# Optimization experiments

Hardware: AMD Instinct MI355X
Metric: run time of the kernel (lower is better)

The kernel has to match this reference:

```python
import jax, jax.numpy as jnp
import numpy as np

B, S, D, E = 2, 2048, 1024, 16  # batch, cutoff (seq), dmodel, n_experts


def setup_inputs() -> dict:
    key = jax.random.key(0)
    k = jax.random.split(key, 6)
    scale = 1.0 / np.sqrt(D)
    return {
        "x": jax.random.normal(k[0], (B, S, D), dtype=jnp.float32),
        "gate": jax.random.normal(k[1], (D, E), dtype=jnp.float32) * scale,
        "W1": jax.random.normal(k[2], (E, D, D), dtype=jnp.float32) * scale,  # lin1: Linear(dmodel, dmodel*E), split per expert
        "b1": jnp.zeros((E, D), dtype=jnp.float32),
        "W2": jax.random.normal(k[3], (E, D, D), dtype=jnp.float32) * scale,  # lin2: Linear(dmodel*E, dmodel), split per expert
        "b2": jnp.zeros((D,), dtype=jnp.float32),
        "topk": 256,
    }


def reference(x, gate, W1, b1, W2, b2, topk):
    # Expert-choice gating: softmax over the token (cutoff) axis per expert.
    logits = jnp.einsum("bsd,de->bse", x, gate)            # (B, S, E)
    probs = jax.nn.softmax(logits, axis=1)                  # softmax over tokens
    # Each expert selects its top-k tokens.
    g, idx = jax.lax.top_k(jnp.swapaxes(probs, 1, 2), topk)  # (B, E, k)
    # Gather selected tokens: (B, E, k, D)
    xin = jnp.take_along_axis(x[:, None, :, :], idx[..., None], axis=2)
    # Per-expert 2-layer FFN (hidden size = dmodel, per width = dmodel*n_experts)
    h = jax.nn.relu(jnp.einsum("bekd,edf->bekf", xin, W1) + b1[None, :, None, :])
    out = jnp.einsum("bekf,efd->bekd", h, W2) + b2           # (B, E, k, D)
    weighted = out * g[..., None]
    # Scatter-add back to token positions.
    y = jnp.zeros_like(x)
    b_idx = jnp.arange(x.shape[0])[:, None, None]            # (B, 1, 1)
    y = y.at[b_idx, idx].add(weighted)
    return y
```

## Files before the change

### kernel.cpp

```cpp
#include <hip/hip_runtime.h>
#include <stdint.h>
#include <math.h>

constexpr int CB = 2;
constexpr int CS = 2048;
constexpr int CD = 1024;
constexpr int CE = 16;
constexpr int CK = 256;

typedef short bf16x8 __attribute__((ext_vector_type(8)));
typedef float f32x4 __attribute__((ext_vector_type(4)));

typedef __attribute__((address_space(1))) const unsigned int gu32;
typedef __attribute__((address_space(3))) unsigned int lu32;

__device__ __forceinline__ void async16(const void* g, void* l) {
    __builtin_amdgcn_global_load_lds((gu32*)g, (lu32*)l, 16, 0, 0);
}

__device__ inline unsigned short f2bf(float f) {
    union { float f; uint32_t u; } v; v.f = f;
    uint32_t u = v.u;
    uint32_t r = (u + 0x7FFFu + ((u >> 16) & 1u)) >> 16;
    return (unsigned short)r;
}

__global__ __launch_bounds__(256)
void logits_kernel(const float* __restrict__ x,
                   const float* __restrict__ gate,
                   float* __restrict__ logits) {
    const int tid = threadIdx.x;
    const int wid = tid >> 6, l = tid & 63;
    const int bs = blockIdx.x * 4 + wid;
    const float* xr = x + (size_t)bs * CD;
    float acc[CE];
#pragma unroll
    for (int e = 0; e < CE; e++) acc[e] = 0.0f;
#pragma unroll
    for (int i = 0; i < 4; i++) {
        const int d0 = i * 256 + l * 4;
        const f32x4 xv = *(const f32x4*)(xr + d0);
#pragma unroll
        for (int j = 0; j < 4; j++) {
            const f32x4* g4 = (const f32x4*)(gate + (size_t)(d0 + j) * CE);
#pragma unroll
            for (int c = 0; c < 4; c++) {
                const f32x4 gv = g4[c];
#pragma unroll
                for (int u = 0; u < 4; u++) acc[c * 4 + u] += xv[j] * gv[u];
            }
        }
    }
#pragma unroll
    for (int e = 0; e < CE; e++) {
        float v = acc[e];
#pragma unroll
        for (int o = 32; o > 0; o >>= 1) v += __shfl_down(v, o);
        if (l == 0) logits[(size_t)bs * CE + e] = v;
    }
}

__global__ void topk_kernel(const float* __restrict__ logits,
                            int* __restrict__ idx_out,
                            float* __restrict__ g_out) {
    const int be = blockIdx.x;
    const int b = be >> 4, e = be & 15;
    const int tid = threadIdx.x;
    const int lane = tid & 63, wid = tid >> 6;

    __shared__ float redf[4];
    __shared__ int hist[256];
    __shared__ int wsum[4];
    __shared__ int sh_bin, sh_rank;
    __shared__ int scnt, eqc;
    __shared__ int eqbuf[CS];

    float lv[8], p[8];
    unsigned int uv[8];
#pragma unroll
    for (int j = 0; j < 8; j++) {
        const int s = tid + j * 256;
        lv[j] = logits[((size_t)(b * CS + s)) * CE + e];
    }
    float m = lv[0];
#pragma unroll
    for (int j = 1; j < 8; j++) m = fmaxf(m, lv[j]);
#pragma unroll
    for (int o = 32; o > 0; o >>= 1) m = fmaxf(m, __shfl_down(m, o));
    if (lane == 0) redf[wid] = m;
    __syncthreads();
    m = fmaxf(fmaxf(redf[0], redf[1]), fmaxf(redf[2], redf[3]));
    __syncthreads();
    float lsum = 0.0f;
#pragma unroll
    for (int j = 0; j < 8; j++) {
        p[j] = expf(lv[j] - m);
        uv[j] = __float_as_uint(p[j]);
        lsum += p[j];
    }
#pragma unroll
    for (int o = 32; o > 0; o >>= 1) lsum += __shfl_down(lsum, o);
    if (lane == 0) redf[wid] = lsum;
    __syncthreads();
    const float total = redf[0] + redf[1] + redf[2] + redf[3];
    const float inv_total = 1.0f / total;

    unsigned int prefix = 0;
    int kneed = CK;
    for (int pass = 0; pass < 4; pass++) {
        const int shift = 24 - 8 * pass;
        __syncthreads();
        hist[tid] = 0;
        __syncthreads();
        const unsigned int hmask = (pass == 0) ? 0u : (0xFFFFFFFFu << (shift + 8));
#pragma unroll
        for (int j = 0; j < 8; j++)
            if ((uv[j] & hmask) == prefix)
                atomicAdd(&hist[(uv[j] >> shift) & 255], 1);
        __syncthreads();
        const int own = hist[tid];
        int s = own;
#pragma unroll
        for (int o = 1; o < 64; o <<= 1) {
            int t = __shfl_down(s, o);
            if (lane + o < 64) s += t;
        }
        if (lane == 0) wsum[wid] = s;
        __syncthreads();
        int above = 0;
        for (int ww = wid + 1; ww < 4; ww++) above += wsum[ww];
        const int incl = s + above;
        if (incl >= kneed && (incl - own) < kneed) {
            sh_bin = tid;
            sh_rank = kneed - (incl - own);
        }
        __syncthreads();
        prefix |= ((unsigned int)sh_bin) << shift;
        kneed = sh_rank;
    }
    const unsigned int v = prefix;
    const int quota = kneed;

    if (tid == 0) { scnt = 0; eqc = 0; }
    __syncthreads();
#pragma unroll
    for (int j = 0; j < 8; j++) {
        const int s = tid + j * 256;
        if (uv[j] > v) {
            const int pos = atomicAdd(&scnt, 1);
            idx_out[be * CK + pos] = s;
            g_out[be * CK + pos] = p[j] * inv_total;
        } else if (uv[j] == v) {
            const int pos = atomicAdd(&eqc, 1);
            eqbuf[pos] = s;
        }
    }
    __syncthreads();
    if (tid == 0) {
        const int cgt = scnt;
        const int n = eqc;
        const float gv = __uint_as_float(v) * inv_total;
        if (n > quota) {
            for (int i = 0; i < quota; i++) {
                int mn = i;
                for (int k2 = i + 1; k2 < n; k2++)
                    if (eqbuf[k2] < eqbuf[mn]) mn = k2;
                const int t2 = eqbuf[i]; eqbuf[i] = eqbuf[mn]; eqbuf[mn] = t2;
            }
        }
        for (int i = 0; i < quota; i++) {
            idx_out[be * CK + cgt + i] = eqbuf[i];
            g_out[be * CK + cgt + i] = gv;
        }
    }
}

__global__ void gather_kernel(const float* __restrict__ x,
                              const int* __restrict__ idx_ws,
                              unsigned short* __restrict__ xinbuf) {
    const int row = blockIdx.x;
    const int be = row >> 8;
    const int b = be >> 4;
    const int tok = idx_ws[row];
    const int c0 = threadIdx.x * 4;
    const f32x4 f = *(const f32x4*)(x + ((size_t)b * CS + tok) * CD + c0);
    union { unsigned short u[4]; uint2 v; } t;
    t.u[0] = f2bf(f[0]); t.u[1] = f2bf(f[1]); t.u[2] = f2bf(f[2]); t.u[3] = f2bf(f[3]);
    *(uint2*)(xinbuf + (size_t)row * CD + c0) = t.v;
}

__global__ __launch_bounds__(256)
void wt_kernel(const float* __restrict__ W, unsigned short* __restrict__ Wt) {
    const int kt = blockIdx.x, nt = blockIdx.y, e = blockIdx.z;
    const float* src = W + (size_t)e * CD * CD;
    unsigned short* dst = Wt + (size_t)e * CD * CD;
    const int tid = threadIdx.x;
    __shared__ unsigned short T[64 * 64];

    const int kr = tid >> 4;
    const int n4 = (tid & 15) << 2;
#pragma unroll
    for (int it = 0; it < 4; it++) {
        const int k = it * 16 + kr;
        const f32x4 v = *(const f32x4*)(src + (size_t)(kt * 64 + k) * CD + nt * 64 + n4);
        const int pp = k >> 4;
        const int klo = k & 15;
#pragma unroll
        for (int i = 0; i < 4; i++) {
            const int n = n4 + i;
            T[n * 64 + ((pp ^ ((n >> 2) & 3)) << 4) + klo] = f2bf(v[i]);
        }
    }
    __syncthreads();
    const int n = tid >> 2;
    const int pp = tid & 3;
    const int sw = pp ^ ((n >> 2) & 3);
    const uint4 a = *(const uint4*)&T[n * 64 + (sw << 4)];
    const uint4 b = *(const uint4*)&T[n * 64 + (sw << 4) + 8];
    unsigned short* drow = dst + (size_t)(nt * 64 + n) * CD + kt * 64 + pp * 16;
    *(uint4*)drow = a;
    *(uint4*)(drow + 8) = b;
}

template <int PHASE>
__global__ __launch_bounds__(256, 4)
void ffn_gemm(const unsigned short* __restrict__ Ain,
              const unsigned short* __restrict__ Wt,
              const float* __restrict__ bias,
              unsigned short* __restrict__ hout,
              const int* __restrict__ idx_ws,
              const float* __restrict__ g_ws,
              float* __restrict__ y) {
    const int mtile = blockIdx.x;
    const int ntile = blockIdx.y;
    const int z = blockIdx.z;
    const int e = z >> 1, b = z & 1;
    const int be = b * 16 + e;
    const int tid = threadIdx.x;
    const int w = tid >> 6, l = tid & 63;
    const int wm = w & 1, wn = w >> 1;
    const int quad = l >> 4, lr = l & 15;

    __shared__ __align__(16) unsigned short As[128 * 64];
    __shared__ __align__(16) unsigned short Bs[64 * 64];

    f32x4 acc[4][2];
    const f32x4 zz = {0.f, 0.f, 0.f, 0.f};
#pragma unroll
    for (int mi = 0; mi < 4; mi++)
#pragma unroll
        for (int ni = 0; ni < 2; ni++) acc[mi][ni] = zz;

    const unsigned short* Abase = Ain + ((size_t)be * CK + mtile * 128) * CD;
    const unsigned short* Bbase = Wt + ((size_t)e * CD + ntile * 64) * CD;

    for (int k0 = 0; k0 < CD; k0 += 64) {
#pragma unroll
        for (int j = 0; j < 4; j++) {
            const int c = (w * 4 + j) * 64 + l;
            const int row = c >> 3;
            const int q = (c & 7) ^ (row & 7);
            async16(Abase + (size_t)row * CD + k0 + q * 8, &As[c * 8]);
        }
#pragma unroll
        for (int j = 0; j < 2; j++) {
            const int c = (w * 2 + j) * 64 + l;
            const int row = c >> 3;
            const int q = (c & 7) ^ (row & 7);
            async16(Bbase + (size_t)row * CD + k0 + q * 8, &Bs[c * 8]);
        }
        __syncthreads();

#pragma unroll
        for (int kk = 0; kk < 2; kk++) {
            bf16x8 af[4], bfr[2];
            const int sq = ((kk * 4 + quad) ^ (lr & 7)) * 8;
#pragma unroll
            for (int mi = 0; mi < 4; mi++)
                af[mi] = *(const bf16x8*)&As[(wm * 64 + mi * 16 + lr) * 64 + sq];
#pragma unroll
            for (int ni = 0; ni < 2; ni++)
                bfr[ni] = *(const bf16x8*)&Bs[(wn * 32 + ni * 16 + lr) * 64 + sq];
#pragma unroll
            for (int mi = 0; mi < 4; mi++)
#pragma unroll
                for (int ni = 0; ni < 2; ni++)
                    acc[mi][ni] = __builtin_amdgcn_mfma_f32_16x16x32_bf16(
                        af[mi], bfr[ni], acc[mi][ni], 0, 0, 0);
        }
        __syncthreads();
    }

    const int gn_base = ntile * 64 + wn * 32;
    if (PHASE == 0) {
#pragma unroll
        for (int mi = 0; mi < 4; mi++)
#pragma unroll
            for (int r = 0; r < 4; r++) {
                const int slot = mtile * 128 + wm * 64 + mi * 16 + quad * 4 + r;
                unsigned short* outrow = hout + ((size_t)be * CK + slot) * CD;
#pragma unroll
                for (int ni = 0; ni < 2; ni++) {
                    const int col = gn_base + ni * 16 + lr;
                    float hv = acc[mi][ni][r] + bias[e * CD + col];
                    hv = fmaxf(hv, 0.0f);
                    outrow[col] = f2bf(hv);
                }
            }
    } else {
#pragma unroll
        for (int mi = 0; mi < 4; mi++)
#pragma unroll
            for (int r = 0; r < 4; r++) {
                const int slot = mtile * 128 + wm * 64 + mi * 16 + quad * 4 + r;
                const int tok = idx_ws[be * CK + slot];
                const float gval = g_ws[be * CK + slot];
                float* yrow = y + ((size_t)b * CS + tok) * CD;
#pragma unroll
                for (int ni = 0; ni < 2; ni++) {
                    const int col = gn_base + ni * 16 + lr;
                    const float val = (acc[mi][ni][r] + bias[col]) * gval;
                    atomicAdd(&yrow[col], val);
                }
            }
    }
}

extern "C" void kernel_launch(void* const* d_in, const int* in_sizes, int n_in,
                              void* d_out, int out_size, void* d_ws, size_t ws_size,
                              hipStream_t stream) {
    const float* x    = (const float*)d_in[0];
    const float* gate = (const float*)d_in[1];
    const float* W1   = (const float*)d_in[2];
    const float* b1   = (const float*)d_in[3];
    const float* W2   = (const float*)d_in[4];
    const float* b2   = (const float*)d_in[5];
    float* y = (float*)d_out;

    char* ws = (char*)d_ws;
    float* logits = (float*)ws;
    int* idxw = (int*)(ws + 262144);
    float* gw = (float*)(ws + 294912);
    unsigned short* xinbuf = (unsigned short*)(ws + 327680);
    unsigned short* hbuf = (unsigned short*)(ws + 17104896);
    unsigned short* wtbuf = (unsigned short*)(ws + 33882112);

    logits_kernel<<<CB * CS / 4, 256, 0, stream>>>(x, gate, logits);
    topk_kernel<<<CB * CE, 256, 0, stream>>>(logits, idxw, gw);
    gather_kernel<<<CB * CE * CK, 256, 0, stream>>>(x, idxw, xinbuf);
    wt_kernel<<<dim3(16, 16, CE), 256, 0, stream>>>(W1, wtbuf);
    hipMemsetAsync(d_out, 0, (size_t)CB * CS * CD * sizeof(float), stream);
    ffn_gemm<0><<<dim3(2, 16, CB * CE), 256, 0, stream>>>(xinbuf, wtbuf, b1, hbuf, idxw, gw, y);
    wt_kernel<<<dim3(16, 16, CE), 256, 0, stream>>>(W2, wtbuf);
    ffn_gemm<1><<<dim3(2, 16, CB * CE), 256, 0, stream>>>(hbuf, wtbuf, b2, nullptr, idxw, gw, y);
}
```

Measured before the change: 316.3 us.

## Split gating logits over D chunks with LDS staging and separate reduction

Replaces the per-token wave logits kernel with a split-K version: each block handles 256 tokens by 64 of the D dimension, staging x through padded LDS and having each thread accumulate all 16 experts for one token. Partial sums are written to a scratch buffer that reuses the hbuf region, and a second kernel reduces them. This removes the per-token cross-lane shuffle reductions, but it adds an extra launch and partial-sum traffic through memory. The logits stage is a small part of the total runtime.

```diff
diff --git a/kernel.cpp b/kernel.cpp
--- a/kernel.cpp
+++ b/kernel.cpp
@@ -26,38 +26,56 @@
 }
 
 __global__ __launch_bounds__(256)
-void logits_kernel(const float* __restrict__ x,
-                   const float* __restrict__ gate,
-                   float* __restrict__ logits) {
+void logits_part_kernel(const float* __restrict__ x,
+                        const float* __restrict__ gate,
+                        float* __restrict__ part) {
+    const int tt = blockIdx.x;
+    const int dt = blockIdx.y;
     const int tid = threadIdx.x;
-    const int wid = tid >> 6, l = tid & 63;
-    const int bs = blockIdx.x * 4 + wid;
-    const float* xr = x + (size_t)bs * CD;
+
+    __shared__ float Xs[256 * 17];
+
     float acc[CE];
 #pragma unroll
     for (int e = 0; e < CE; e++) acc[e] = 0.0f;
-#pragma unroll
-    for (int i = 0; i < 4; i++) {
-        const int d0 = i * 256 + l * 4;
-        const f32x4 xv = *(const f32x4*)(xr + d0);
-#pragma unroll
-        for (int j = 0; j < 4; j++) {
-            const f32x4* g4 = (const f32x4*)(gate + (size_t)(d0 + j) * CE);
-#pragma unroll
-            for (int c = 0; c < 4; c++) {
-                const f32x4 gv = g4[c];
-#pragma unroll
-                for (int u = 0; u < 4; u++) acc[c * 4 + u] += xv[j] * gv[u];
-            }
-        }
-    }
-#pragma unroll
-    for (int e = 0; e < CE; e++) {
-        float v = acc[e];
-#pragma unroll
-        for (int o = 32; o > 0; o >>= 1) v += __shfl_down(v, o);
-        if (l == 0) logits[(size_t)bs * CE + e] = v;
-    }
+
+    const int tokl = tid >> 2;
+    const int c4 = (tid & 3) << 2;
+
+    for (int dch = 0; dch < 4; dch++) {
+        const int dbase = dt * 64 + dch * 16;
+        __syncthreads();
+#pragma unroll
+        for (int q = 0; q < 4; q++) {
+            const int tok = q * 64 + tokl;
+            const f32x4 v = *(const f32x4*)(x + ((size_t)(tt * 256 + tok)) * CD + dbase + c4);
+            Xs[tok * 17 + c4 + 0] = v[0];
+            Xs[tok * 17 + c4 + 1] = v[1];
+            Xs[tok * 17 + c4 + 2] = v[2];
+            Xs[tok * 17 + c4 + 3] = v[3];
+        }
+        __syncthreads();
+#pragma unroll
+        for (int d = 0; d < 16; d++) {
+            const float xv = Xs[tid * 17 + d];
+            const float* gr = gate + (size_t)(dbase + d) * CE;
+#pragma unroll
+            for (int e = 0; e < CE; e++) acc[e] = fmaf(xv, gr[e], acc[e]);
+        }
+    }
+    float* pr = part + ((size_t)dt * (CB * CS) + tt * 256 + tid) * CE;
+#pragma unroll
+    for (int e = 0; e < CE; e++) pr[e] = acc[e];
+}
+
+__global__ __launch_bounds__(256)
+void logits_reduce_kernel(const float* __restrict__ part,
+                          float* __restrict__ logits) {
+    const int i = blockIdx.x * 256 + threadIdx.x;
+    float s = 0.0f;
+#pragma unroll
+    for (int p = 0; p < 16; p++) s += part[(size_t)p * (CB * CS * CE) + i];
+    logits[i] = s;
 }
 
 __global__ void topk_kernel(const float* __restrict__ logits,
@@ -343,9 +361,11 @@
     float* gw = (float*)(ws + 294912);
     unsigned short* xinbuf = (unsigned short*)(ws + 327680);
     unsigned short* hbuf = (unsigned short*)(ws + 17104896);
+    float* partbuf = (float*)(ws + 17104896);
     unsigned short* wtbuf = (unsigned short*)(ws + 33882112);
 
-    logits_kernel<<<CB * CS / 4, 256, 0, stream>>>(x, gate, logits);
+    logits_part_kernel<<<dim3(16, 16), 256, 0, stream>>>(x, gate, partbuf);
+    logits_reduce_kernel<<<CB * CS * CE / 256, 256, 0, stream>>>(partbuf, logits);
     topk_kernel<<<CB * CE, 256, 0, stream>>>(logits, idxw, gw);
     gather_kernel<<<CB * CE * CK, 256, 0, stream>>>(x, idxw, xinbuf);
     wt_kernel<<<dim3(16, 16, CE), 256, 0, stream>>>(W1, wtbuf);
```

New measurement: 291.1 us. 8.0% less time.
